# Optimization experiments

Hardware: AMD Instinct MI355X
Metric: run time of the kernel (lower is better)

## Reference

```python
import jax, jax.numpy as jnp
import numpy as np

HEADS = 4
BN_EPS = 1e-5


def _linear_attention(x, heads):
    # x: [B, L, C]; per-head linear attention: softmax(Q,dim=feat) @ (softmax(K,dim=seq)^T @ V)
    B, L, C = x.shape
    dh = C // heads
    h = x.reshape(B, L, heads, dh)
    q = jax.nn.softmax(h, axis=-1)          # softmax over feature dim (dim=2 in torch)
    k = jax.nn.softmax(h, axis=1)           # softmax over sequence dim (dim=1 in torch)
    kv = jnp.einsum('blhd,blhe->bhde', k, h)   # [B, H, dh, dh]
    out = jnp.einsum('blhd,bhde->blhe', q, kv) # [B, L, H, dh]
    return out.reshape(B, L, C)


def setup_inputs() -> dict:
    key = jax.random.key(0)
    ks = jax.random.split(key, 10)
    B, C, L, DOUT, NB = 32, 32, 16384, 10, 3
    s = 0.1
    return {
        'x': jax.random.normal(ks[0], (B, C, L), jnp.float32),
        'fcW1': jax.random.normal(ks[1], (NB, C, C), jnp.float32) * s,
        'fcb1': jax.random.normal(ks[2], (NB, C), jnp.float32) * s,
        'fcW2': jax.random.normal(ks[3], (NB, C, C), jnp.float32) * s,
        'fcb2': jax.random.normal(ks[4], (NB, C), jnp.float32) * s,
        'Wh': jax.random.normal(ks[5], (C, C), jnp.float32) * s,
        'bh': jax.random.normal(ks[6], (C,), jnp.float32) * s,
        'bn_gamma': jnp.ones((C,), jnp.float32),
        'bn_beta': jnp.zeros((C,), jnp.float32),
        'bn_mean': jnp.zeros((C,), jnp.float32),
        'bn_var': jnp.ones((C,), jnp.float32),
        'Wf': jax.random.normal(ks[7], (C, DOUT), jnp.float32) * s,
        'bf': jax.random.normal(ks[8], (DOUT,), jnp.float32) * s,
    }


def reference(x, fcW1, fcb1, fcW2, fcb2, Wh, bh, bn_gamma, bn_beta, bn_mean, bn_var, Wf, bf):
    gelu = lambda t: jax.nn.gelu(t, approximate=False)  # torch default GELU is exact erf
    h = jnp.transpose(x, (0, 2, 1))  # [B, C, L] -> [B, L, C]
    n_blocks = fcW1.shape[0]
    for i in range(n_blocks):
        h = _linear_attention(h, HEADS)
        h = gelu(h @ fcW1[i] + fcb1[i])
        h = gelu(h @ fcW2[i] + fcb2[i])
    pooled = jnp.mean(h, axis=1)  # AdaptiveAvgPool1d(1) over L -> [B, C]
    y = pooled @ Wh + bh
    y = (y - bn_mean) * jax.lax.rsqrt(bn_var + BN_EPS) * bn_gamma + bn_beta  # BatchNorm1d (eval)
    y = gelu(y)
    return y @ Wf + bf
```

## Files before the change

### kernel.cpp

```cpp
#include <hip/hip_runtime.h>
#include <cstddef>

#define B_ 32
#define C_ 32
#define L_ 16384
#define H_ 4
#define DH_ 8
#define NB_ 3
#define DOUT_ 10
#define SEG_ 512
#define S_ (L_/SEG_)

#define TILE 256
#define AST  40
#define OST  260

typedef _Float16 f16_t;
typedef _Float16 f16x2 __attribute__((ext_vector_type(2)));
typedef _Float16 f16x8 __attribute__((ext_vector_type(8)));
typedef float    f32x4 __attribute__((ext_vector_type(4)));

__device__ __forceinline__ float gelu_f(float x){
    const float z  = fabsf(x) * 0.70710678118654752440f;
    const float t  = __builtin_amdgcn_rcpf(fmaf(0.3275911f, z, 1.0f));
    const float e  = __expf(-z * z);
    float p = fmaf(t, 1.061405429f, -1.453152027f);
    p = fmaf(t, p, 1.421413741f);
    p = fmaf(t, p, -0.284496736f);
    p = fmaf(t, p, 0.254829592f);
    const float erfz = 1.0f - p * t * e;
    const float phi  = fmaf(copysignf(erfz, x), 0.5f, 0.5f);
    return x * phi;
}

#define RED_MAX32(v) do{ v = fmaxf(v, __shfl_xor(v,1));  v = fmaxf(v, __shfl_xor(v,2)); \
                         v = fmaxf(v, __shfl_xor(v,4));  v = fmaxf(v, __shfl_xor(v,8)); \
                         v = fmaxf(v, __shfl_xor(v,16)); }while(0)
#define RED_SUM32(v) do{ v += __shfl_xor(v,1);  v += __shfl_xor(v,2); \
                         v += __shfl_xor(v,4);  v += __shfl_xor(v,8); \
                         v += __shfl_xor(v,16); }while(0)

__global__ __launch_bounds__(256) void stats_kernel(const float* __restrict__ h,
                                                    float* __restrict__ part){
    const int seg = blockIdx.x;
    const int hd  = blockIdx.y;
    const int b   = blockIdx.z;
    const int t   = threadIdx.x;
    const int d   = t >> 5;
    const int j   = t & 31;

    __shared__ float tile[8][SEG_];
    __shared__ float sm[8];

    const float* hb = h + (size_t)b * ((size_t)C_*L_) + (size_t)(hd*DH_)*L_ + (size_t)seg*SEG_;

    for (int f = t; f < 8*SEG_/4; f += 256){
        const int row = f >> 7;
        const int c4  = (f & 127) << 2;
        *(f32x4*)&tile[row][c4] = *(const f32x4*)&hb[(size_t)row*L_ + c4];
    }
    __syncthreads();

    float m = -INFINITY;
    #pragma unroll
    for (int i = 0; i < SEG_/32; i++) m = fmaxf(m, tile[d][j + 32*i]);
    RED_MAX32(m);
    if (j == 0) sm[d] = m;
    const float m_d = m;

    float s = 0.0f;
    float kv[8];
    #pragma unroll
    for (int e = 0; e < 8; e++) kv[e] = 0.0f;
    #pragma unroll
    for (int i = 0; i < SEG_/32; i++){
        const int k = j + 32*i;
        const float ek = __expf(tile[d][k] - m_d);
        s += ek;
        #pragma unroll
        for (int e = 0; e < 8; e++) kv[e] = fmaf(ek, tile[e][k], kv[e]);
    }
    RED_SUM32(s);
    #pragma unroll
    for (int e = 0; e < 8; e++){ RED_SUM32(kv[e]); }
    __syncthreads();

    float* po = part + (size_t)((b*H_ + hd)*S_ + seg) * 80;
    if (j == 0){
        po[8 + d] = s;
        #pragma unroll
        for (int e = 0; e < 8; e++) po[16 + d*8 + e] = kv[e];
    }
    if (t < 8) po[t] = sm[t];
}

template<bool LAST>
__global__ __launch_bounds__(256)
__attribute__((amdgpu_waves_per_eu(3, 4)))
void block_kernel(const float* hin,
                  float* hout,
                  const float* __restrict__ part,
                  const float* __restrict__ W1,
                  const float* __restrict__ b1,
                  const float* __restrict__ W2,
                  const float* __restrict__ b2,
                  float* __restrict__ pooled){
    __shared__ __align__(16) char AObuf[TILE*AST*2];
    f16_t* const Ash = (f16_t*)AObuf;
    float* const O16 = (float*)AObuf;
    __shared__ f16_t Bsh1[32*AST];
    __shared__ f16_t Bsh2[32*AST];
    __shared__ float sb1[32], sb2[32];
    __shared__ float kvsh[256];
    __shared__ float pool[32];

    const int tid = threadIdx.x;
    const int b   = blockIdx.y;
    const int l0  = blockIdx.x * TILE;
    const int l   = l0 + tid;
    const size_t base = (size_t)b * ((size_t)C_*L_);

    float h[32];
    #pragma unroll
    for (int c = 0; c < 32; c++) h[c] = hin[base + (size_t)c*L_ + l];

    for (int i = tid; i < 1024; i += 256){
        const int k = i >> 5, n = i & 31;
        Bsh1[n*AST + k] = (f16_t)W1[i];
        Bsh2[n*AST + k] = (f16_t)W2[i];
    }
    if (tid < 32){ sb1[tid] = b1[tid]; sb2[tid] = b2[tid]; }
    if (LAST && tid < 32) pool[tid] = 0.0f;

    {
        const int hh_t = tid >> 6;
        const int tt   = tid & 63;
        const int dd   = tt >> 3;
        const float* pp = part + (size_t)(b*H_ + hh_t) * S_ * 80;
        float M = -INFINITY;
        for (int s2 = 0; s2 < S_; s2++) M = fmaxf(M, pp[s2*80 + dd]);
        float ssum = 0.0f, kvs = 0.0f;
        for (int s2 = 0; s2 < S_; s2++){
            const float sc = __expf(pp[s2*80 + dd] - M);
            ssum = fmaf(pp[s2*80 + 8  + dd], sc, ssum);
            kvs  = fmaf(pp[s2*80 + 16 + tt], sc, kvs);
        }
        kvsh[tid] = kvs / ssum;
    }
    __syncthreads();

    float attn[32];
    #pragma unroll
    for (int hh = 0; hh < 4; hh++){
        float mq = h[hh*8];
        #pragma unroll
        for (int d2 = 1; d2 < 8; d2++) mq = fmaxf(mq, h[hh*8 + d2]);
        float es[8]; float qs = 0.f;
        #pragma unroll
        for (int d2 = 0; d2 < 8; d2++){ es[d2] = __expf(h[hh*8 + d2] - mq); qs += es[d2]; }
        const float inv = __builtin_amdgcn_rcpf(qs);
        #pragma unroll
        for (int e = 0; e < 8; e++){
            float a = 0.f;
            #pragma unroll
            for (int d2 = 0; d2 < 8; d2++) a += es[d2] * kvsh[hh*64 + d2*8 + e];
            attn[hh*8 + e] = a * inv;
        }
    }

    #pragma unroll
    for (int k2 = 0; k2 < 32; k2 += 2){
        f16x2 pr = { (f16_t)attn[k2], (f16_t)attn[k2+1] };
        *(f16x2*)&Ash[tid*AST + k2] = pr;
    }
    __syncthreads();

    const int wv   = tid >> 6;
    const int lane = tid & 63;
    const int lr   = lane & 15;
    const int lk   = lane >> 4;
    const f32x4 zero = {0.f, 0.f, 0.f, 0.f};

    f16x8 a[4], bw[2];
    f32x4 d[8];

    #pragma unroll
    for (int mt = 0; mt < 4; mt++)
        a[mt] = *(const f16x8*)&Ash[(wv*64 + mt*16 + lr)*AST + lk*8];
    #pragma unroll
    for (int nt = 0; nt < 2; nt++)
        bw[nt] = *(const f16x8*)&Bsh1[(nt*16 + lr)*AST + lk*8];
    #pragma unroll
    for (int nt = 0; nt < 2; nt++)
        #pragma unroll
        for (int mt = 0; mt < 4; mt++)
            d[nt*4+mt] = __builtin_amdgcn_mfma_f32_16x16x32_f16(a[mt], bw[nt], zero, 0, 0, 0);

    #pragma unroll
    for (int nt = 0; nt < 2; nt++){
        const float bias = sb1[nt*16 + lr];
        #pragma unroll
        for (int mt = 0; mt < 4; mt++){
            #pragma unroll
            for (int r = 0; r < 4; r++){
                const float v = gelu_f(d[nt*4+mt][r] + bias);
                Ash[(wv*64 + mt*16 + lk*4 + r)*AST + (nt*16 + lr)] = (f16_t)v;
            }
        }
    }
    __syncthreads();

    #pragma unroll
    for (int mt = 0; mt < 4; mt++)
        a[mt] = *(const f16x8*)&Ash[(wv*64 + mt*16 + lr)*AST + lk*8];
    #pragma unroll
    for (int nt = 0; nt < 2; nt++)
        bw[nt] = *(const f16x8*)&Bsh2[(nt*16 + lr)*AST + lk*8];
    #pragma unroll
    for (int nt = 0; nt < 2; nt++)
        #pragma unroll
        for (int mt = 0; mt < 4; mt++)
            d[nt*4+mt] = __builtin_amdgcn_mfma_f32_16x16x32_f16(a[mt], bw[nt], zero, 0, 0, 0);

    #pragma unroll
    for (int nt = 0; nt < 2; nt++){
        const float bias = sb2[nt*16 + lr];
        #pragma unroll
        for (int mt = 0; mt < 4; mt++)
            #pragma unroll
            for (int r = 0; r < 4; r++)
                d[nt*4+mt][r] = gelu_f(d[nt*4+mt][r] + bias);
    }

    if (!LAST){
        #pragma unroll
        for (int nt = 0; nt < 2; nt++){
            __syncthreads();
            #pragma unroll
            for (int mt = 0; mt < 4; mt++)
                *(f32x4*)&O16[lr*OST + wv*64 + mt*16 + lk*4] = d[nt*4+mt];
            __syncthreads();
            #pragma unroll
            for (int c = 0; c < 16; c++)
                hout[base + (size_t)(nt*16 + c)*L_ + l0 + tid] = O16[c*OST + tid];
        }
    } else {
        __syncthreads();
        #pragma unroll
        for (int nt = 0; nt < 2; nt++){
            float ps = 0.f;
            #pragma unroll
            for (int mt = 0; mt < 4; mt++)
                ps += d[nt*4+mt][0] + d[nt*4+mt][1] + d[nt*4+mt][2] + d[nt*4+mt][3];
            atomicAdd(&pool[nt*16 + lr], ps);
        }
        __syncthreads();
        if (tid < 32) atomicAdd(&pooled[b*32 + tid], pool[tid]);
    }
}

__global__ __launch_bounds__(1024) void head_kernel(const float* __restrict__ pooled,
                                                    const float* __restrict__ Wh,
                                                    const float* __restrict__ bh,
                                                    const float* __restrict__ gam,
                                                    const float* __restrict__ bet,
                                                    const float* __restrict__ mean,
                                                    const float* __restrict__ var,
                                                    const float* __restrict__ Wf,
                                                    const float* __restrict__ bf,
                                                    float* __restrict__ out){
    __shared__ float y2[32][32];
    const int t = threadIdx.x;
    const int b = t >> 5, c = t & 31;
    float a = bh[c];
    const float invL = 1.0f / (float)L_;
    #pragma unroll
    for (int d = 0; d < 32; d++) a += (pooled[b*32 + d] * invL) * Wh[d*32 + c];
    a = (a - mean[c]) * rsqrtf(var[c] + 1e-5f) * gam[c] + bet[c];
    y2[b][c] = gelu_f(a);
    __syncthreads();
    if (t < B_*DOUT_){
        const int b2 = t / DOUT_, j = t % DOUT_;
        float r = bf[j];
        #pragma unroll
        for (int c2 = 0; c2 < 32; c2++) r += y2[b2][c2] * Wf[c2*DOUT_ + j];
        out[t] = r;
    }
}

extern "C" void kernel_launch(void* const* d_in, const int* in_sizes, int n_in,
                              void* d_out, int out_size, void* d_ws, size_t ws_size,
                              hipStream_t stream){
    (void)in_sizes; (void)n_in; (void)out_size; (void)ws_size;
    const float* x    = (const float*)d_in[0];
    const float* fW1  = (const float*)d_in[1];
    const float* fb1  = (const float*)d_in[2];
    const float* fW2  = (const float*)d_in[3];
    const float* fb2  = (const float*)d_in[4];
    const float* Wh   = (const float*)d_in[5];
    const float* bh   = (const float*)d_in[6];
    const float* gam  = (const float*)d_in[7];
    const float* bet  = (const float*)d_in[8];
    const float* mean = (const float*)d_in[9];
    const float* var  = (const float*)d_in[10];
    const float* Wf   = (const float*)d_in[11];
    const float* bf   = (const float*)d_in[12];
    float* out = (float*)d_out;

    float* hbuf   = (float*)d_ws;
    float* part   = hbuf + (size_t)B_*C_*L_;
    float* pooled = part + (size_t)B_*H_*S_*80;

    hipMemsetAsync(pooled, 0, B_*C_*sizeof(float), stream);

    dim3 sgrid(S_, H_, B_);
    dim3 bgrid(L_/TILE, B_);

    stats_kernel<<<sgrid, 256, 0, stream>>>(x, part);
    block_kernel<false><<<bgrid, 256, 0, stream>>>(x, hbuf, part,
        fW1, fb1, fW2, fb2, nullptr);
    stats_kernel<<<sgrid, 256, 0, stream>>>(hbuf, part);
    block_kernel<false><<<bgrid, 256, 0, stream>>>(hbuf, hbuf, part,
        fW1 + C_*C_, fb1 + C_, fW2 + C_*C_, fb2 + C_, nullptr);
    stats_kernel<<<sgrid, 256, 0, stream>>>(hbuf, part);
    block_kernel<true><<<bgrid, 256, 0, stream>>>(hbuf, nullptr, part,
        fW1 + 2*C_*C_, fb1 + 2*C_, fW2 + 2*C_*C_, fb2 + 2*C_, pooled);

    head_kernel<<<1, 1024, 0, stream>>>(pooled, Wh, bh, gam, bet, mean, var, Wf, bf, out);
}
```

Baseline: 294.1 us.

## Store intermediate activations in fp16, shorten GELU polynomial, drop syncs and memset

Intermediate activations between blocks are now stored in fp16 rather than fp32, which halves the global read and write traffic of the stats and block kernels. The GELU erf approximation switches to a shorter 3-term polynomial. Several __syncthreads are removed, and the output is written straight from MFMA registers as f16x4 instead of being transposed through shared memory. The pooled-buffer memset is folded into a stats kernel. The risks are reduced accuracy from fp16 storage and the coarser erf, and possible shared-memory races: each thread writes Ash rows that other lanes in the same wave read, and the barrier before the MFMA reads is gone.

```diff
diff --git a/kernel.cpp b/kernel.cpp
--- a/kernel.cpp
+++ b/kernel.cpp
@@ -13,21 +13,19 @@
 
 #define TILE 256
 #define AST  40
-#define OST  260
 
 typedef _Float16 f16_t;
 typedef _Float16 f16x2 __attribute__((ext_vector_type(2)));
+typedef _Float16 f16x4 __attribute__((ext_vector_type(4)));
 typedef _Float16 f16x8 __attribute__((ext_vector_type(8)));
 typedef float    f32x4 __attribute__((ext_vector_type(4)));
 
 __device__ __forceinline__ float gelu_f(float x){
     const float z  = fabsf(x) * 0.70710678118654752440f;
-    const float t  = __builtin_amdgcn_rcpf(fmaf(0.3275911f, z, 1.0f));
+    const float t  = __builtin_amdgcn_rcpf(fmaf(0.47047f, z, 1.0f));
     const float e  = __expf(-z * z);
-    float p = fmaf(t, 1.061405429f, -1.453152027f);
-    p = fmaf(t, p, 1.421413741f);
-    p = fmaf(t, p, -0.284496736f);
-    p = fmaf(t, p, 0.254829592f);
+    float p = fmaf(t, 0.7478556f, -0.0958798f);
+    p = fmaf(t, p, 0.3480242f);
     const float erfz = 1.0f - p * t * e;
     const float phi  = fmaf(copysignf(erfz, x), 0.5f, 0.5f);
     return x * phi;
@@ -40,8 +38,10 @@
                          v += __shfl_xor(v,4);  v += __shfl_xor(v,8); \
                          v += __shfl_xor(v,16); }while(0)
 
-__global__ __launch_bounds__(256) void stats_kernel(const float* __restrict__ h,
-                                                    float* __restrict__ part){
+template<typename T>
+__global__ __launch_bounds__(256) void stats_kernel(const T* __restrict__ h,
+                                                    float* __restrict__ part,
+                                                    float* __restrict__ zpool){
     const int seg = blockIdx.x;
     const int hd  = blockIdx.y;
     const int b   = blockIdx.z;
@@ -52,12 +52,27 @@
     __shared__ float tile[8][SEG_];
     __shared__ float sm[8];
 
-    const float* hb = h + (size_t)b * ((size_t)C_*L_) + (size_t)(hd*DH_)*L_ + (size_t)seg*SEG_;
-
-    for (int f = t; f < 8*SEG_/4; f += 256){
-        const int row = f >> 7;
-        const int c4  = (f & 127) << 2;
-        *(f32x4*)&tile[row][c4] = *(const f32x4*)&hb[(size_t)row*L_ + c4];
+    if (zpool != nullptr && blockIdx.x == 0 && blockIdx.y == 0 && blockIdx.z == 0)
+        for (int i = t; i < B_*C_; i += 256) zpool[i] = 0.0f;
+
+    const T* hb = h + (size_t)b * ((size_t)C_*L_) + (size_t)(hd*DH_)*L_ + (size_t)seg*SEG_;
+
+    if constexpr (sizeof(T) == 4){
+        for (int f = t; f < 8*SEG_/4; f += 256){
+            const int row = f >> 7;
+            const int c4  = (f & 127) << 2;
+            *(f32x4*)&tile[row][c4] = *(const f32x4*)&hb[(size_t)row*L_ + c4];
+        }
+    } else {
+        for (int f = t; f < 8*SEG_/8; f += 256){
+            const int row = f >> 6;
+            const int c8  = (f & 63) << 3;
+            const f16x8 v = *(const f16x8*)&hb[(size_t)row*L_ + c8];
+            f32x4 lo = {(float)v[0], (float)v[1], (float)v[2], (float)v[3]};
+            f32x4 hi = {(float)v[4], (float)v[5], (float)v[6], (float)v[7]};
+            *(f32x4*)&tile[row][c8]     = lo;
+            *(f32x4*)&tile[row][c8 + 4] = hi;
+        }
     }
     __syncthreads();
 
@@ -94,20 +109,18 @@
     if (t < 8) po[t] = sm[t];
 }
 
-template<bool LAST>
+template<bool FIRST, bool LAST>
 __global__ __launch_bounds__(256)
 __attribute__((amdgpu_waves_per_eu(3, 4)))
-void block_kernel(const float* hin,
-                  float* hout,
+void block_kernel(const void* hin,
+                  f16_t* hout,
                   const float* __restrict__ part,
                   const float* __restrict__ W1,
                   const float* __restrict__ b1,
                   const float* __restrict__ W2,
                   const float* __restrict__ b2,
                   float* __restrict__ pooled){
-    __shared__ __align__(16) char AObuf[TILE*AST*2];
-    f16_t* const Ash = (f16_t*)AObuf;
-    float* const O16 = (float*)AObuf;
+    __shared__ __align__(16) f16_t Ash[TILE*AST];
     __shared__ f16_t Bsh1[32*AST];
     __shared__ f16_t Bsh2[32*AST];
     __shared__ float sb1[32], sb2[32];
@@ -121,8 +134,15 @@
     const size_t base = (size_t)b * ((size_t)C_*L_);
 
     float h[32];
-    #pragma unroll
-    for (int c = 0; c < 32; c++) h[c] = hin[base + (size_t)c*L_ + l];
+    if constexpr (FIRST){
+        const float* hf = (const float*)hin;
+        #pragma unroll
+        for (int c = 0; c < 32; c++) h[c] = hf[base + (size_t)c*L_ + l];
+    } else {
+        const f16_t* hh = (const f16_t*)hin;
+        #pragma unroll
+        for (int c = 0; c < 32; c++) h[c] = (float)hh[base + (size_t)c*L_ + l];
+    }
 
     for (int i = tid; i < 1024; i += 256){
         const int k = i >> 5, n = i & 31;
@@ -173,7 +193,6 @@
         f16x2 pr = { (f16_t)attn[k2], (f16_t)attn[k2+1] };
         *(f16x2*)&Ash[tid*AST + k2] = pr;
     }
-    __syncthreads();
 
     const int wv   = tid >> 6;
     const int lane = tid & 63;
@@ -200,15 +219,13 @@
     for (int nt = 0; nt < 2; nt++){
         const float bias = sb1[nt*16 + lr];
         #pragma unroll
-        for (int mt = 0; mt < 4; mt++){
+        for (int mt = 0; mt < 4; mt++)
             #pragma unroll
             for (int r = 0; r < 4; r++){
                 const float v = gelu_f(d[nt*4+mt][r] + bias);
                 Ash[(wv*64 + mt*16 + lk*4 + r)*AST + (nt*16 + lr)] = (f16_t)v;
             }
-        }
-    }
-    __syncthreads();
+    }
 
     #pragma unroll
     for (int mt = 0; mt < 4; mt++)
@@ -234,18 +251,15 @@
 
     if (!LAST){
         #pragma unroll
-        for (int nt = 0; nt < 2; nt++){
-            __syncthreads();
-            #pragma unroll
-            for (int mt = 0; mt < 4; mt++)
-                *(f32x4*)&O16[lr*OST + wv*64 + mt*16 + lk*4] = d[nt*4+mt];
-            __syncthreads();
-            #pragma unroll
-            for (int c = 0; c < 16; c++)
-                hout[base + (size_t)(nt*16 + c)*L_ + l0 + tid] = O16[c*OST + tid];
-        }
+        for (int nt = 0; nt < 2; nt++)
+            #pragma unroll
+            for (int mt = 0; mt < 4; mt++){
+                const f32x4 dv = d[nt*4+mt];
+                f16x4 hv = { (f16_t)dv[0], (f16_t)dv[1], (f16_t)dv[2], (f16_t)dv[3] };
+                *(f16x4*)&hout[base + (size_t)(nt*16 + lr)*L_
+                               + l0 + wv*64 + mt*16 + lk*4] = hv;
+            }
     } else {
-        __syncthreads();
         #pragma unroll
         for (int nt = 0; nt < 2; nt++){
             float ps = 0.f;
@@ -307,23 +321,21 @@
     const float* bf   = (const float*)d_in[12];
     float* out = (float*)d_out;
 
-    float* hbuf   = (float*)d_ws;
-    float* part   = hbuf + (size_t)B_*C_*L_;
+    f16_t* hbuf   = (f16_t*)d_ws;
+    float* part   = (float*)((char*)d_ws + (size_t)B_*C_*L_*2);
     float* pooled = part + (size_t)B_*H_*S_*80;
-
-    hipMemsetAsync(pooled, 0, B_*C_*sizeof(float), stream);
 
     dim3 sgrid(S_, H_, B_);
     dim3 bgrid(L_/TILE, B_);
 
-    stats_kernel<<<sgrid, 256, 0, stream>>>(x, part);
-    block_kernel<false><<<bgrid, 256, 0, stream>>>(x, hbuf, part,
+    stats_kernel<float><<<sgrid, 256, 0, stream>>>(x, part, nullptr);
+    block_kernel<true, false><<<bgrid, 256, 0, stream>>>(x, hbuf, part,
         fW1, fb1, fW2, fb2, nullptr);
-    stats_kernel<<<sgrid, 256, 0, stream>>>(hbuf, part);
-    block_kernel<false><<<bgrid, 256, 0, stream>>>(hbuf, hbuf, part,
+    stats_kernel<f16_t><<<sgrid, 256, 0, stream>>>(hbuf, part, nullptr);
+    block_kernel<false, false><<<bgrid, 256, 0, stream>>>(hbuf, hbuf, part,
         fW1 + C_*C_, fb1 + C_, fW2 + C_*C_, fb2 + C_, nullptr);
-    stats_kernel<<<sgrid, 256, 0, stream>>>(hbuf, part);
-    block_kernel<true><<<bgrid, 256, 0, stream>>>(hbuf, nullptr, part,
+    stats_kernel<f16_t><<<sgrid, 256, 0, stream>>>(hbuf, part, pooled);
+    block_kernel<false, true><<<bgrid, 256, 0, stream>>>(hbuf, nullptr, part,
         fW1 + 2*C_*C_, fb1 + 2*C_, fW2 + 2*C_*C_, fb2 + 2*C_, pooled);
 
     head_kernel<<<1, 1024, 0, stream>>>(pooled, Wh, bh, gam, bet, mean, var, Wf, bf, out);
```

New measurement: 276.4 us. 6.0% less time.
